# Optimization experiments

Hardware: AMD Instinct MI355X
Metric: run time of the kernel (lower is better)

The kernel has to match this reference:

```python
import jax, jax.numpy as jnp
import numpy as np
from jax import lax

ALPHA = 5.0   # ATan surrogate alpha
TAU = 2.0     # LIF tau
HEADS = 16
SCALE = 0.25

@jax.custom_vjp
def atan_spike(x):
    return (x >= 0.0).astype(x.dtype)

def _atan_fwd(x):
    return atan_spike(x), x

def _atan_bwd(x, g):
    # spikingjelly surrogate.ATan: d/dx = alpha/2 / (1 + (pi/2*alpha*x)^2)
    return (g * (ALPHA / 2.0) / (1.0 + (jnp.pi / 2.0 * ALPHA * x) ** 2),)

atan_spike.defvjp(_atan_fwd, _atan_bwd)

def lif(x, v_th=1.0):
    # Multi-step LIF, hard reset to 0, detach_reset=True. x: [T, ...]
    def step(v, xt):
        h = v + (xt - v) / TAU
        s = atan_spike(h - v_th)
        v_new = h * (1.0 - lax.stop_gradient(s))
        return v_new, s
    _, spikes = lax.scan(step, jnp.zeros_like(x[0]), x)
    return spikes

def conv_bn(x, w, gamma, beta, mean, var, eps=1e-5):
    # 1x1 Conv1d (bias=False) + BatchNorm1d (eval stats). x: [..., C, N]
    y = jnp.einsum('oc,...cn->...on', w, x)
    scale = gamma * lax.rsqrt(var + eps)
    return y * scale[:, None] + (beta - mean * scale)[:, None]

def setup_inputs() -> dict:
    key = jax.random.key(0)
    ks = jax.random.split(key, 22)
    T, B, C, H, W = 4, 8, 256, 32, 16
    d = {}
    d['x'] = jax.random.normal(ks[0], (T, B, C, H, W), jnp.float32)
    i = 1
    for n in ['q', 'k', 'v', 'proj']:
        d[n + '_w'] = jax.random.normal(ks[i], (C, C), jnp.float32) / 16.0; i += 1
        d[n + '_gamma'] = jax.random.uniform(ks[i], (C,), jnp.float32, 0.5, 1.5); i += 1
        d[n + '_beta'] = jax.random.normal(ks[i], (C,), jnp.float32) * 0.1; i += 1
        d[n + '_mean'] = jax.random.normal(ks[i], (C,), jnp.float32) * 0.1; i += 1
        d[n + '_var'] = jax.random.uniform(ks[i], (C,), jnp.float32, 0.5, 1.5); i += 1
    return d

def reference(x, q_w, q_gamma, q_beta, q_mean, q_var,
              k_w, k_gamma, k_beta, k_mean, k_var,
              v_w, v_gamma, v_beta, v_mean, v_var,
              proj_w, proj_gamma, proj_beta, proj_mean, proj_var):
    T, B, C, H, W = x.shape
    N = H * W
    hd = C // HEADS
    xf = x.reshape(T, B, C, N)

    def branch(w, g, b, m, v):
        s = lif(conv_bn(xf, w, g, b, m, v))  # [T,B,C,N] binary spikes
        # -> [T,B,heads,N,head_dim]
        return s.transpose(0, 1, 3, 2).reshape(T, B, N, HEADS, hd).transpose(0, 1, 3, 2, 4)

    q = branch(q_w, q_gamma, q_beta, q_mean, q_var)
    k = branch(k_w, k_gamma, k_beta, k_mean, k_var)
    v = branch(v_w, v_gamma, v_beta, v_mean, v_var)

    attn = jnp.einsum('tbhnd,tbhmd->tbhnm', q, k)           # binary q@k^T
    y = jnp.einsum('tbhnm,tbhmd->tbhnd', attn, v) * SCALE   # (attn @ v) * 0.25
    y = y.transpose(0, 1, 2, 4, 3).reshape(T, B, C, N)       # transpose(3,4) then merge heads

    # attn_lif is applied on flatten(0,1): time dim = T*B (faithful to source)
    s = lif(y.reshape(T * B, C, N), v_th=0.5)
    p = conv_bn(s, proj_w, proj_gamma, proj_beta, proj_mean, proj_var)
    out = lif(p.reshape(T, B, C, W, H))  # note W,H swap, as in source
    return out
```

## Files before the change

kernel.cpp:

```cpp
#include <hip/hip_runtime.h>

#define TT 4
#define BB 8
#define CC 256
#define NN 512
#define HEADS 16
#define HD 16

#define GLL16(gp, lp) \
    __builtin_amdgcn_global_load_lds( \
        (const __attribute__((address_space(1))) void*)(gp), \
        (__attribute__((address_space(3))) void*)(lp), 16, 0, 0)

struct WPtrs  { const float* w[4]; };
struct BnPtrs { const float* g[4]; const float* b[4]; const float* m[4]; const float* v[4]; };

__global__ __launch_bounds__(256)
void prep_bn(BnPtrs p, float* __restrict__ sc, float* __restrict__ bi)
{
    int m = blockIdx.x, c = threadIdx.x;
    float rs = __fdiv_rn(1.0f, __fsqrt_rn(__fadd_rn(p.v[m][c], 1e-5f)));
    float s  = __fmul_rn(p.g[m][c], rs);
    sc[m * CC + c] = s;
    bi[m * CC + c] = __fsub_rn(p.b[m][c], __fmul_rn(p.m[m][c], s));
}

__global__ __launch_bounds__(256)
void transpose_w(WPtrs p, float* __restrict__ wt)
{
    __shared__ float t[16][17];
    const int m  = blockIdx.z;
    const float* w = p.w[m];
    const int o0 = blockIdx.y * 16, k0 = blockIdx.x * 16;
    const int tx = threadIdx.x, ty = threadIdx.y;
    t[ty][tx] = w[(size_t)(o0 + ty) * CC + k0 + tx];
    __syncthreads();
    wt[(size_t)m * CC * CC + (size_t)(k0 + ty) * CC + o0 + tx] = t[tx][ty];
}

__global__ __launch_bounds__(256)
void qkv_conv_bn_lif_pack(const float* __restrict__ x,
                          const float* __restrict__ wt,
                          const float* __restrict__ scA,
                          const float* __restrict__ biA,
                          unsigned long long* __restrict__ bits)
{
    __shared__ float WtS[64][64];
    __shared__ float Xs[64][64];
    __shared__ unsigned short Spk[64][16];

    const int tid = threadIdx.x;
    const int tx = tid & 15;
    const int ty = tid >> 4;
    const int br = blockIdx.z >> 3;
    const int b  = blockIdx.z & 7;
    const int o0 = blockIdx.y * 64;
    const int n0 = blockIdx.x * 64;

    const float* wtb = wt + (size_t)br * CC * CC;
    unsigned long long* bout = bits + (size_t)br * (TT * BB * CC * 8);

    float sc[4], bi[4];
#pragma unroll
    for (int i = 0; i < 4; ++i) {
        sc[i] = scA[br * CC + o0 + ty * 4 + i];
        bi[i] = biA[br * CC + o0 + ty * 4 + i];
    }

    float vst[4][4];
#pragma unroll
    for (int i = 0; i < 4; ++i)
#pragma unroll
        for (int j = 0; j < 4; ++j) vst[i][j] = 0.0f;

    for (int t = 0; t < TT; ++t) {
        float acc[4][4];
#pragma unroll
        for (int i = 0; i < 4; ++i)
#pragma unroll
            for (int j = 0; j < 4; ++j) acc[i][j] = 0.0f;

        const float* xb = x + (size_t)(t * BB + b) * CC * NN;

        for (int k0 = 0; k0 < CC; k0 += 64) {
            __syncthreads();
#pragma unroll
            for (int i = 0; i < 4; ++i) {
                int idx = tid + 256 * i;
                int row = idx >> 4;
                int cg  = idx & 15;
                GLL16(&wtb[(size_t)(k0 + row) * CC + o0 + cg * 4], &WtS[row][cg * 4]);
                GLL16(&xb [(size_t)(k0 + row) * NN + n0 + cg * 4], &Xs [row][cg * 4]);
            }
            __syncthreads();
#pragma unroll 8
            for (int kk = 0; kk < 64; ++kk) {
                float4 wv = *reinterpret_cast<const float4*>(&WtS[kk][ty * 4]);
                float4 xv = *reinterpret_cast<const float4*>(&Xs[kk][tx * 4]);
#pragma unroll
                for (int i = 0; i < 4; ++i) {
                    float wvi = (i == 0) ? wv.x : (i == 1) ? wv.y : (i == 2) ? wv.z : wv.w;
                    acc[i][0] = __fmaf_rn(wvi, xv.x, acc[i][0]);
                    acc[i][1] = __fmaf_rn(wvi, xv.y, acc[i][1]);
                    acc[i][2] = __fmaf_rn(wvi, xv.z, acc[i][2]);
                    acc[i][3] = __fmaf_rn(wvi, xv.w, acc[i][3]);
                }
            }
        }

        unsigned int nib[4] = {0u, 0u, 0u, 0u};
#pragma unroll
        for (int i = 0; i < 4; ++i) {
#pragma unroll
            for (int j = 0; j < 4; ++j) {
                float ybn = __fadd_rn(__fmul_rn(acc[i][j], sc[i]), bi[i]);
                float h   = __fadd_rn(vst[i][j],
                                      __fmul_rn(__fsub_rn(ybn, vst[i][j]), 0.5f));
                bool sp = (h >= 1.0f);
                vst[i][j] = sp ? 0.0f : h;
                nib[i] |= (sp ? 1u : 0u) << j;
            }
        }
        __syncthreads();
#pragma unroll
        for (int i = 0; i < 4; ++i) Spk[ty * 4 + i][tx] = (unsigned short)nib[i];
        __syncthreads();
        if (tid < 64) {
            unsigned long long m = 0ULL;
#pragma unroll
            for (int g = 0; g < 16; ++g)
                m |= (unsigned long long)(Spk[tid][g] & 0xF) << (4 * g);
            bout[((size_t)(t * BB + b) * CC + o0 + tid) * 8 + blockIdx.x] = m;
        }
    }
}

__global__ __launch_bounds__(256)
void attn_kernel(const unsigned long long* __restrict__ bq,
                 const unsigned long long* __restrict__ bk,
                 const unsigned long long* __restrict__ bv,
                 float* __restrict__ y)
{
    const int blk = blockIdx.x;
    const int h  = blk & 15;
    const int tb = blk >> 4;
    const int tid = threadIdx.x;

    __shared__ unsigned long long kb[16][8], vb[16][8], qb[16][8];
    __shared__ float M[16][16];

    size_t base = ((size_t)tb * CC + h * HD) * 8;
    if (tid < 128) {
        int j = tid >> 3, ch = tid & 7;
        kb[j][ch] = bk[base + j * 8 + ch];
        vb[j][ch] = bv[base + j * 8 + ch];
        qb[j][ch] = bq[base + j * 8 + ch];
    }
    __syncthreads();

    {
        int j = tid >> 4, d = tid & 15;
        int cnt = 0;
#pragma unroll
        for (int ch = 0; ch < 8; ++ch)
            cnt += __popcll(kb[j][ch] & vb[d][ch]);
        M[j][d] = (float)cnt;
    }
    __syncthreads();

    size_t ybase = ((size_t)tb * CC + h * HD) * (size_t)NN;
#pragma unroll
    for (int r = 0; r < 2; ++r) {
        int n = tid + 256 * r;
        int ch = n >> 6, sh = n & 63;
        float acc[16];
#pragma unroll
        for (int d = 0; d < 16; ++d) acc[d] = 0.0f;
#pragma unroll
        for (int j = 0; j < 16; ++j) {
            float bit = (float)((qb[j][ch] >> sh) & 1ULL);
#pragma unroll
            for (int d = 0; d < 16; ++d)
                acc[d] = __fmaf_rn(bit, M[j][d], acc[d]);
        }
#pragma unroll
        for (int d = 0; d < 16; ++d)
            y[ybase + (size_t)d * NN + n] = __fmul_rn(acc[d], 0.25f);
    }
}

__global__ __launch_bounds__(256)
void attn_lif(const float* __restrict__ y, unsigned char* __restrict__ s)
{
    const int e4 = blockIdx.x * 256 + threadIdx.x;
    float4 v = make_float4(0.f, 0.f, 0.f, 0.f);
    for (int tb = 0; tb < 32; ++tb) {
        float4 xv = *reinterpret_cast<const float4*>(&y[(size_t)tb * (CC * NN) + e4 * 4]);
        uchar4 o;
        float h;
        h = __fadd_rn(v.x, __fmul_rn(__fsub_rn(xv.x, v.x), 0.5f));
        o.x = (h >= 0.5f) ? 1 : 0; v.x = (h >= 0.5f) ? 0.0f : h;
        h = __fadd_rn(v.y, __fmul_rn(__fsub_rn(xv.y, v.y), 0.5f));
        o.y = (h >= 0.5f) ? 1 : 0; v.y = (h >= 0.5f) ? 0.0f : h;
        h = __fadd_rn(v.z, __fmul_rn(__fsub_rn(xv.z, v.z), 0.5f));
        o.z = (h >= 0.5f) ? 1 : 0; v.z = (h >= 0.5f) ? 0.0f : h;
        h = __fadd_rn(v.w, __fmul_rn(__fsub_rn(xv.w, v.w), 0.5f));
        o.w = (h >= 0.5f) ? 1 : 0; v.w = (h >= 0.5f) ? 0.0f : h;
        *reinterpret_cast<uchar4*>(&s[(size_t)tb * (CC * NN) + e4 * 4]) = o;
    }
}

__global__ __launch_bounds__(256)
void proj_bn_lif(const unsigned char* __restrict__ s,
                 const float* __restrict__ wt,
                 const float* __restrict__ scA,
                 const float* __restrict__ biA,
                 float* __restrict__ out)
{
    __shared__ float WtS[64][64];
    __shared__ float Xs[64][36];

    const int tid = threadIdx.x;
    const int tx = tid & 15;
    const int ty = tid >> 4;
    const int b  = blockIdx.z;
    const int o0 = blockIdx.y * 64;
    const int n0 = blockIdx.x * 32;

    float sc[4], bi[4];
#pragma unroll
    for (int i = 0; i < 4; ++i) {
        sc[i] = scA[3 * CC + o0 + ty * 4 + i];
        bi[i] = biA[3 * CC + o0 + ty * 4 + i];
    }

    float vst[4][2];
#pragma unroll
    for (int i = 0; i < 4; ++i) { vst[i][0] = 0.0f; vst[i][1] = 0.0f; }

    for (int t = 0; t < TT; ++t) {
        float acc[4][2];
#pragma unroll
        for (int i = 0; i < 4; ++i) { acc[i][0] = 0.0f; acc[i][1] = 0.0f; }

        const unsigned char* sb = s + (size_t)(t * BB + b) * CC * NN;

        for (int k0 = 0; k0 < CC; k0 += 64) {
            __syncthreads();
#pragma unroll
            for (int i = 0; i < 4; ++i) {
                int idx = tid + 256 * i;
                int row = idx >> 4, cg = idx & 15;
                GLL16(&wt[(size_t)(k0 + row) * CC + o0 + cg * 4], &WtS[row][cg * 4]);
            }
#pragma unroll
            for (int i = 0; i < 2; ++i) {
                int idx = tid + 256 * i;
                int row = idx >> 3, seg = idx & 7;
                uchar4 u = *reinterpret_cast<const uchar4*>(
                    &sb[(size_t)(k0 + row) * NN + n0 + seg * 4]);
                float4 f = make_float4((float)u.x, (float)u.y, (float)u.z, (float)u.w);
                *reinterpret_cast<float4*>(&Xs[row][seg * 4]) = f;
            }
            __syncthreads();
#pragma unroll 8
            for (int kk = 0; kk < 64; ++kk) {
                float4 wv = *reinterpret_cast<const float4*>(&WtS[kk][ty * 4]);
                float2 xv = *reinterpret_cast<const float2*>(&Xs[kk][tx * 2]);
#pragma unroll
                for (int i = 0; i < 4; ++i) {
                    float wvi = (i == 0) ? wv.x : (i == 1) ? wv.y : (i == 2) ? wv.z : wv.w;
                    acc[i][0] = __fmaf_rn(wvi, xv.x, acc[i][0]);
                    acc[i][1] = __fmaf_rn(wvi, xv.y, acc[i][1]);
                }
            }
        }

#pragma unroll
        for (int i = 0; i < 4; ++i) {
            float2 o2;
            float r[2];
#pragma unroll
            for (int j = 0; j < 2; ++j) {
                float ybn = __fadd_rn(__fmul_rn(acc[i][j], sc[i]), bi[i]);
                float h   = __fadd_rn(vst[i][j],
                                      __fmul_rn(__fsub_rn(ybn, vst[i][j]), 0.5f));
                bool sp = (h >= 1.0f);
                vst[i][j] = sp ? 0.0f : h;
                r[j] = sp ? 1.0f : 0.0f;
            }
            o2.x = r[0]; o2.y = r[1];
            *reinterpret_cast<float2*>(
                &out[((size_t)(t * BB + b) * CC + o0 + ty * 4 + i) * NN + n0 + tx * 2]) = o2;
        }
    }
}

extern "C" void kernel_launch(void* const* d_in, const int* in_sizes, int n_in,
                              void* d_out, int out_size, void* d_ws, size_t ws_size,
                              hipStream_t stream) {
    const float* x = (const float*)d_in[0];

    WPtrs wp;
    BnPtrs bp;
    for (int m = 0; m < 4; ++m) {
        wp.w[m] = (const float*)d_in[1 + m * 5 + 0];
        bp.g[m] = (const float*)d_in[1 + m * 5 + 1];
        bp.b[m] = (const float*)d_in[1 + m * 5 + 2];
        bp.m[m] = (const float*)d_in[1 + m * 5 + 3];
        bp.v[m] = (const float*)d_in[1 + m * 5 + 4];
    }

    char* ws = (char*)d_ws;
    float* wt   = (float*)ws;
    float* scA  = (float*)(ws + (1u << 20));
    float* biA  = (float*)(ws + (1u << 20) + 4096);
    unsigned long long* bits = (unsigned long long*)(ws + (1u << 20) + 8192);
    float* ybuf = (float*)(ws + (1u << 20) + 8192 + (1536u << 10));
    unsigned char* sbuf = (unsigned char*)(ws + (1u << 20) + 8192 + (1536u << 10) + (16u << 20));

    prep_bn<<<4, 256, 0, stream>>>(bp, scA, biA);
    transpose_w<<<dim3(16, 16, 4), dim3(16, 16), 0, stream>>>(wp, wt);

    qkv_conv_bn_lif_pack<<<dim3(8, 4, 24), 256, 0, stream>>>(x, wt, scA, biA, bits);

    const unsigned long long* bq = bits;
    const unsigned long long* bk = bits + 65536;
    const unsigned long long* bv = bits + 131072;
    attn_kernel<<<512, 256, 0, stream>>>(bq, bk, bv, ybuf);
    attn_lif<<<128, 256, 0, stream>>>(ybuf, sbuf);
    proj_bn_lif<<<dim3(16, 4, 8), 256, 0, stream>>>(sbuf, wt + 3 * CC * CC, scA, biA, (float*)d_out);
}
```

Baseline: 263.9 us.

## Double-buffer LDS staging in conv GEMMs and write attn LIF spikes in place

Both the QKV and projection conv kernels now run one flattened loop over time and 32-wide K stages with double-buffered LDS. The next stage's global-to-LDS load is issued before the current stage is computed, leaving one barrier per stage, and the 4 spike nibbles are packed together at the end. attn_lif now handles one element per thread across 512 blocks, preloading all 32 steps into registers and writing float spikes back into the y buffer in place. This lets the projection kernel load its input directly to LDS instead of converting bytes to floats. The trade-off is 4x more spike traffic than the byte buffer, plus extra register pressure from the launch-bounds occupancy hint.

```diff
diff --git a/kernel.cpp b/kernel.cpp
--- a/kernel.cpp
+++ b/kernel.cpp
@@ -38,15 +38,15 @@
     wt[(size_t)m * CC * CC + (size_t)(k0 + ty) * CC + o0 + tx] = t[tx][ty];
 }
 
-__global__ __launch_bounds__(256)
+__global__ __launch_bounds__(256, 4)
 void qkv_conv_bn_lif_pack(const float* __restrict__ x,
                           const float* __restrict__ wt,
                           const float* __restrict__ scA,
                           const float* __restrict__ biA,
                           unsigned long long* __restrict__ bits)
 {
-    __shared__ float WtS[64][64];
-    __shared__ float Xs[64][64];
+    __shared__ float W2[2][32][64];
+    __shared__ float X2[2][32][64];
     __shared__ unsigned short Spk[64][16];
 
     const int tid = threadIdx.x;
@@ -67,69 +67,82 @@
         bi[i] = biA[br * CC + o0 + ty * 4 + i];
     }
 
+    auto stage = [&](int s, int buf) {
+        const int t  = s >> 3;
+        const int k0 = (s & 7) * 32;
+        const float* xb = x + (size_t)(t * BB + b) * CC * NN;
+#pragma unroll
+        for (int i = 0; i < 2; ++i) {
+            int idx = tid + 256 * i;
+            int row = idx >> 4;
+            int cg  = idx & 15;
+            GLL16(&wtb[(size_t)(k0 + row) * CC + o0 + cg * 4], &W2[buf][row][cg * 4]);
+            GLL16(&xb [(size_t)(k0 + row) * NN + n0 + cg * 4], &X2[buf][row][cg * 4]);
+        }
+    };
+
     float vst[4][4];
+    float acc[4][4];
+    unsigned int tnib[4] = {0u, 0u, 0u, 0u};
 #pragma unroll
     for (int i = 0; i < 4; ++i)
 #pragma unroll
-        for (int j = 0; j < 4; ++j) vst[i][j] = 0.0f;
-
-    for (int t = 0; t < TT; ++t) {
-        float acc[4][4];
-#pragma unroll
-        for (int i = 0; i < 4; ++i)
-#pragma unroll
-            for (int j = 0; j < 4; ++j) acc[i][j] = 0.0f;
-
-        const float* xb = x + (size_t)(t * BB + b) * CC * NN;
-
-        for (int k0 = 0; k0 < CC; k0 += 64) {
-            __syncthreads();
+        for (int j = 0; j < 4; ++j) { vst[i][j] = 0.0f; acc[i][j] = 0.0f; }
+
+    stage(0, 0);
+    __syncthreads();
+
+    int cur = 0;
+    for (int s = 0; s < 32; ++s) {
+        if (s < 31) stage(s + 1, cur ^ 1);
+
+#pragma unroll 8
+        for (int kk = 0; kk < 32; ++kk) {
+            float4 wv = *reinterpret_cast<const float4*>(&W2[cur][kk][ty * 4]);
+            float4 xv = *reinterpret_cast<const float4*>(&X2[cur][kk][tx * 4]);
 #pragma unroll
             for (int i = 0; i < 4; ++i) {
-                int idx = tid + 256 * i;
-                int row = idx >> 4;
-                int cg  = idx & 15;
-                GLL16(&wtb[(size_t)(k0 + row) * CC + o0 + cg * 4], &WtS[row][cg * 4]);
-                GLL16(&xb [(size_t)(k0 + row) * NN + n0 + cg * 4], &Xs [row][cg * 4]);
+                float wvi = (i == 0) ? wv.x : (i == 1) ? wv.y : (i == 2) ? wv.z : wv.w;
+                acc[i][0] = __fmaf_rn(wvi, xv.x, acc[i][0]);
+                acc[i][1] = __fmaf_rn(wvi, xv.y, acc[i][1]);
+                acc[i][2] = __fmaf_rn(wvi, xv.z, acc[i][2]);
+                acc[i][3] = __fmaf_rn(wvi, xv.w, acc[i][3]);
             }
-            __syncthreads();
-#pragma unroll 8
-            for (int kk = 0; kk < 64; ++kk) {
-                float4 wv = *reinterpret_cast<const float4*>(&WtS[kk][ty * 4]);
-                float4 xv = *reinterpret_cast<const float4*>(&Xs[kk][tx * 4]);
-#pragma unroll
-                for (int i = 0; i < 4; ++i) {
-                    float wvi = (i == 0) ? wv.x : (i == 1) ? wv.y : (i == 2) ? wv.z : wv.w;
-                    acc[i][0] = __fmaf_rn(wvi, xv.x, acc[i][0]);
-                    acc[i][1] = __fmaf_rn(wvi, xv.y, acc[i][1]);
-                    acc[i][2] = __fmaf_rn(wvi, xv.z, acc[i][2]);
-                    acc[i][3] = __fmaf_rn(wvi, xv.w, acc[i][3]);
+        }
+
+        if ((s & 7) == 7) {
+            const int t = s >> 3;
+#pragma unroll
+            for (int i = 0; i < 4; ++i) {
+                unsigned int nib = 0u;
+#pragma unroll
+                for (int j = 0; j < 4; ++j) {
+                    float ybn = __fadd_rn(__fmul_rn(acc[i][j], sc[i]), bi[i]);
+                    float h   = __fadd_rn(vst[i][j],
+                                          __fmul_rn(__fsub_rn(ybn, vst[i][j]), 0.5f));
+                    bool sp = (h >= 1.0f);
+                    vst[i][j] = sp ? 0.0f : h;
+                    nib |= (sp ? 1u : 0u) << j;
+                    acc[i][j] = 0.0f;
                 }
+                tnib[i] |= nib << (4 * t);
             }
         }
 
-        unsigned int nib[4] = {0u, 0u, 0u, 0u};
-#pragma unroll
-        for (int i = 0; i < 4; ++i) {
-#pragma unroll
-            for (int j = 0; j < 4; ++j) {
-                float ybn = __fadd_rn(__fmul_rn(acc[i][j], sc[i]), bi[i]);
-                float h   = __fadd_rn(vst[i][j],
-                                      __fmul_rn(__fsub_rn(ybn, vst[i][j]), 0.5f));
-                bool sp = (h >= 1.0f);
-                vst[i][j] = sp ? 0.0f : h;
-                nib[i] |= (sp ? 1u : 0u) << j;
-            }
-        }
         __syncthreads();
-#pragma unroll
-        for (int i = 0; i < 4; ++i) Spk[ty * 4 + i][tx] = (unsigned short)nib[i];
-        __syncthreads();
-        if (tid < 64) {
+        cur ^= 1;
+    }
+
+#pragma unroll
+    for (int i = 0; i < 4; ++i) Spk[ty * 4 + i][tx] = (unsigned short)tnib[i];
+    __syncthreads();
+    if (tid < 64) {
+#pragma unroll
+        for (int t = 0; t < 4; ++t) {
             unsigned long long m = 0ULL;
 #pragma unroll
             for (int g = 0; g < 16; ++g)
-                m |= (unsigned long long)(Spk[tid][g] & 0xF) << (4 * g);
+                m |= (unsigned long long)((Spk[tid][g] >> (4 * t)) & 0xF) << (4 * g);
             bout[((size_t)(t * BB + b) * CC + o0 + tid) * 8 + blockIdx.x] = m;
         }
     }
@@ -190,35 +203,32 @@
 }
 
 __global__ __launch_bounds__(256)
-void attn_lif(const float* __restrict__ y, unsigned char* __restrict__ s)
-{
-    const int e4 = blockIdx.x * 256 + threadIdx.x;
-    float4 v = make_float4(0.f, 0.f, 0.f, 0.f);
+void attn_lif(float* __restrict__ y)
+{
+    const int e = blockIdx.x * 256 + threadIdx.x;
+    float xs[32];
+#pragma unroll
+    for (int tb = 0; tb < 32; ++tb)
+        xs[tb] = y[(size_t)tb * (CC * NN) + e];
+    float v = 0.0f;
+#pragma unroll
     for (int tb = 0; tb < 32; ++tb) {
-        float4 xv = *reinterpret_cast<const float4*>(&y[(size_t)tb * (CC * NN) + e4 * 4]);
-        uchar4 o;
-        float h;
-        h = __fadd_rn(v.x, __fmul_rn(__fsub_rn(xv.x, v.x), 0.5f));
-        o.x = (h >= 0.5f) ? 1 : 0; v.x = (h >= 0.5f) ? 0.0f : h;
-        h = __fadd_rn(v.y, __fmul_rn(__fsub_rn(xv.y, v.y), 0.5f));
-        o.y = (h >= 0.5f) ? 1 : 0; v.y = (h >= 0.5f) ? 0.0f : h;
-        h = __fadd_rn(v.z, __fmul_rn(__fsub_rn(xv.z, v.z), 0.5f));
-        o.z = (h >= 0.5f) ? 1 : 0; v.z = (h >= 0.5f) ? 0.0f : h;
-        h = __fadd_rn(v.w, __fmul_rn(__fsub_rn(xv.w, v.w), 0.5f));
-        o.w = (h >= 0.5f) ? 1 : 0; v.w = (h >= 0.5f) ? 0.0f : h;
-        *reinterpret_cast<uchar4*>(&s[(size_t)tb * (CC * NN) + e4 * 4]) = o;
-    }
-}
-
-__global__ __launch_bounds__(256)
-void proj_bn_lif(const unsigned char* __restrict__ s,
+        float h = __fadd_rn(v, __fmul_rn(__fsub_rn(xs[tb], v), 0.5f));
+        bool sp = (h >= 0.5f);
+        y[(size_t)tb * (CC * NN) + e] = sp ? 1.0f : 0.0f;
+        v = sp ? 0.0f : h;
+    }
+}
+
+__global__ __launch_bounds__(256, 4)
+void proj_bn_lif(const float* __restrict__ sfl,
                  const float* __restrict__ wt,
                  const float* __restrict__ scA,
                  const float* __restrict__ biA,
                  float* __restrict__ out)
 {
-    __shared__ float WtS[64][64];
-    __shared__ float Xs[64][36];
+    __shared__ float W2[2][32][64];
+    __shared__ float X2[2][32][32];
 
     const int tid = threadIdx.x;
     const int tx = tid & 15;
@@ -234,65 +244,72 @@
         bi[i] = biA[3 * CC + o0 + ty * 4 + i];
     }
 
-    float vst[4][2];
-#pragma unroll
-    for (int i = 0; i < 4; ++i) { vst[i][0] = 0.0f; vst[i][1] = 0.0f; }
-
-    for (int t = 0; t < TT; ++t) {
-        float acc[4][2];
-#pragma unroll
-        for (int i = 0; i < 4; ++i) { acc[i][0] = 0.0f; acc[i][1] = 0.0f; }
-
-        const unsigned char* sb = s + (size_t)(t * BB + b) * CC * NN;
-
-        for (int k0 = 0; k0 < CC; k0 += 64) {
-            __syncthreads();
+    auto stage = [&](int s, int buf) {
+        const int t  = s >> 3;
+        const int k0 = (s & 7) * 32;
+        const float* sb = sfl + (size_t)(t * BB + b) * CC * NN;
+#pragma unroll
+        for (int i = 0; i < 2; ++i) {
+            int idx = tid + 256 * i;
+            int row = idx >> 4, cg = idx & 15;
+            GLL16(&wt[(size_t)(k0 + row) * CC + o0 + cg * 4], &W2[buf][row][cg * 4]);
+        }
+        {
+            int row = tid >> 3, cg = tid & 7;
+            GLL16(&sb[(size_t)(k0 + row) * NN + n0 + cg * 4], &X2[buf][row][cg * 4]);
+        }
+    };
+
+    float vst[4][2], acc[4][2];
+#pragma unroll
+    for (int i = 0; i < 4; ++i) {
+        vst[i][0] = 0.0f; vst[i][1] = 0.0f;
+        acc[i][0] = 0.0f; acc[i][1] = 0.0f;
+    }
+
+    stage(0, 0);
+    __syncthreads();
+
+    int cur = 0;
+    for (int s = 0; s < 32; ++s) {
+        if (s < 31) stage(s + 1, cur ^ 1);
+
+#pragma unroll 8
+        for (int kk = 0; kk < 32; ++kk) {
+            float4 wv = *reinterpret_cast<const float4*>(&W2[cur][kk][ty * 4]);
+            float2 xv = *reinterpret_cast<const float2*>(&X2[cur][kk][tx * 2]);
 #pragma unroll
             for (int i = 0; i < 4; ++i) {
-                int idx = tid + 256 * i;
-                int row = idx >> 4, cg = idx & 15;
-                GLL16(&wt[(size_t)(k0 + row) * CC + o0 + cg * 4], &WtS[row][cg * 4]);
+                float wvi = (i == 0) ? wv.x : (i == 1) ? wv.y : (i == 2) ? wv.z : wv.w;
+                acc[i][0] = __fmaf_rn(wvi, xv.x, acc[i][0]);
+                acc[i][1] = __fmaf_rn(wvi, xv.y, acc[i][1]);
             }
-#pragma unroll
-            for (int i = 0; i < 2; ++i) {
-                int idx = tid + 256 * i;
-                int row = idx >> 3, seg = idx & 7;
-                uchar4 u = *reinterpret_cast<const uchar4*>(
-                    &sb[(size_t)(k0 + row) * NN + n0 + seg * 4]);
-                float4 f = make_float4((float)u.x, (float)u.y, (float)u.z, (float)u.w);
-                *reinterpret_cast<float4*>(&Xs[row][seg * 4]) = f;
+        }
+
+        if ((s & 7) == 7) {
+            const int t = s >> 3;
+#pragma unroll
+            for (int i = 0; i < 4; ++i) {
+                float2 o2;
+                float r[2];
+#pragma unroll
+                for (int j = 0; j < 2; ++j) {
+                    float ybn = __fadd_rn(__fmul_rn(acc[i][j], sc[i]), bi[i]);
+                    float h   = __fadd_rn(vst[i][j],
+                                          __fmul_rn(__fsub_rn(ybn, vst[i][j]), 0.5f));
+                    bool sp = (h >= 1.0f);
+                    vst[i][j] = sp ? 0.0f : h;
+                    r[j] = sp ? 1.0f : 0.0f;
+                    acc[i][j] = 0.0f;
+                }
+                o2.x = r[0]; o2.y = r[1];
+                *reinterpret_cast<float2*>(
+                    &out[((size_t)(t * BB + b) * CC + o0 + ty * 4 + i) * NN + n0 + tx * 2]) = o2;
             }
-            __syncthreads();
-#pragma unroll 8
-            for (int kk = 0; kk < 64; ++kk) {
-                float4 wv = *reinterpret_cast<const float4*>(&WtS[kk][ty * 4]);
-                float2 xv = *reinterpret_cast<const float2*>(&Xs[kk][tx * 2]);
-#pragma unroll
-                for (int i = 0; i < 4; ++i) {
-                    float wvi = (i == 0) ? wv.x : (i == 1) ? wv.y : (i == 2) ? wv.z : wv.w;
-                    acc[i][0] = __fmaf_rn(wvi, xv.x, acc[i][0]);
-                    acc[i][1] = __fmaf_rn(wvi, xv.y, acc[i][1]);
-                }
-            }
-        }
-
-#pragma unroll
-        for (int i = 0; i < 4; ++i) {
-            float2 o2;
-            float r[2];
-#pragma unroll
-            for (int j = 0; j < 2; ++j) {
-                float ybn = __fadd_rn(__fmul_rn(acc[i][j], sc[i]), bi[i]);
-                float h   = __fadd_rn(vst[i][j],
-                                      __fmul_rn(__fsub_rn(ybn, vst[i][j]), 0.5f));
-                bool sp = (h >= 1.0f);
-                vst[i][j] = sp ? 0.0f : h;
-                r[j] = sp ? 1.0f : 0.0f;
-            }
-            o2.x = r[0]; o2.y = r[1];
-            *reinterpret_cast<float2*>(
-                &out[((size_t)(t * BB + b) * CC + o0 + ty * 4 + i) * NN + n0 + tx * 2]) = o2;
-        }
+        }
+
+        __syncthreads();
+        cur ^= 1;
     }
 }
 
@@ -317,7 +334,6 @@
     float* biA  = (float*)(ws + (1u << 20) + 4096);
     unsigned long long* bits = (unsigned long long*)(ws + (1u << 20) + 8192);
     float* ybuf = (float*)(ws + (1u << 20) + 8192 + (1536u << 10));
-    unsigned char* sbuf = (unsigned char*)(ws + (1u << 20) + 8192 + (1536u << 10) + (16u << 20));
 
     prep_bn<<<4, 256, 0, stream>>>(bp, scA, biA);
     transpose_w<<<dim3(16, 16, 4), dim3(16, 16), 0, stream>>>(wp, wt);
@@ -328,6 +344,6 @@
     const unsigned long long* bk = bits + 65536;
     const unsigned long long* bv = bits + 131072;
     attn_kernel<<<512, 256, 0, stream>>>(bq, bk, bv, ybuf);
-    attn_lif<<<128, 256, 0, stream>>>(ybuf, sbuf);
-    proj_bn_lif<<<dim3(16, 4, 8), 256, 0, stream>>>(sbuf, wt + 3 * CC * CC, scA, biA, (float*)d_out);
-}
+    attn_lif<<<512, 256, 0, stream>>>(ybuf);
+    proj_bn_lif<<<dim3(16, 4, 8), 256, 0, stream>>>(ybuf, wt + 3 * CC * CC, scA, biA, (float*)d_out);
+}
```

Result: no change. 266.8 us (+1.1%).
